# Optimization experiments

Hardware: AMD Instinct MI355X
Metric: run time of the kernel (lower is better)

The kernel has to match this reference:

```python
import jax, jax.numpy as jnp
import numpy as np
import math

B, S, D_EMB = 1, 4096, 768
N_HEADS, D_QKV = 12, 64
INV_TEMP = 1.0


def setup_inputs() -> dict:
    key = jax.random.key(0)
    ks = jax.random.split(key, 11)
    s = 0.02
    return {
        "q_in": jax.random.normal(ks[0], (B, S, D_EMB), jnp.float32),
        "k_in": jax.random.normal(ks[1], (B, S, D_EMB), jnp.float32),
        "v_in": jax.random.normal(ks[2], (B, S, D_EMB), jnp.float32),
        "W_q": jax.random.normal(ks[3], (D_EMB, N_HEADS * D_QKV), jnp.float32) * s,
        "b_q": jnp.zeros((N_HEADS * D_QKV,), jnp.float32),
        "W_k": jax.random.normal(ks[4], (D_EMB, N_HEADS * D_QKV), jnp.float32) * s,
        "b_k": jnp.zeros((N_HEADS * D_QKV,), jnp.float32),
        "W_v": jax.random.normal(ks[5], (D_EMB, N_HEADS * D_QKV), jnp.float32) * s,
        "b_v": jnp.zeros((N_HEADS * D_QKV,), jnp.float32),
        "W_o": jax.random.normal(ks[6], (N_HEADS * D_QKV, D_EMB), jnp.float32) * s,
        "b_o": jnp.zeros((D_EMB,), jnp.float32),
    }


def _split_heads(x):  # [B,S,H*D] -> [B,H,S,D]
    b, s, _ = x.shape
    return x.reshape(b, s, N_HEADS, D_QKV).transpose(0, 2, 1, 3)


def reference(q_in, k_in, v_in, W_q, b_q, W_k, b_k, W_v, b_v, W_o, b_o):
    q = _split_heads(q_in @ W_q + b_q)
    k = _split_heads(k_in @ W_k + b_k)
    v = _split_heads(v_in @ W_v + b_v)
    # full [B,H,S,S] score matrix (module materializes it for custom masking)
    scores = INV_TEMP * jnp.einsum('bhqd,bhkd->bhqk', q, k) / math.sqrt(D_QKV)
    attn = jax.nn.softmax(scores, axis=-1)
    out = jnp.einsum('bhqk,bhkd->bhqd', attn, v)  # [B,H,S,D]
    out = out.transpose(0, 2, 1, 3).reshape(q_in.shape[0], q_in.shape[1], N_HEADS * D_QKV)
    return out @ W_o + b_o
```

## Files before the change

### kernel.cpp

```cpp
#include <hip/hip_runtime.h>

#define S 4096
#define E 768
#define NH 12
#define DH 64
#define QSCALE (0.125f * 1.44269504f)

typedef __bf16 bf16;
typedef __bf16 bf16x4 __attribute__((ext_vector_type(4)));
typedef __bf16 bf16x8 __attribute__((ext_vector_type(8)));
typedef float  f32x4  __attribute__((ext_vector_type(4)));

__device__ __forceinline__ void async16(const bf16* g, bf16* l) {
  __builtin_amdgcn_global_load_lds(
      (const __attribute__((address_space(1))) void*)g,
      (__attribute__((address_space(3))) void*)l, 16, 0, 0);
}

__global__ __launch_bounds__(256) void cast3(const float* __restrict__ i0,
                                             const float* __restrict__ i1,
                                             const float* __restrict__ i2,
                                             bf16* __restrict__ o0,
                                             bf16* __restrict__ o1,
                                             bf16* __restrict__ o2) {
  const float* in = blockIdx.z == 0 ? i0 : (blockIdx.z == 1 ? i1 : i2);
  bf16* out = blockIdx.z == 0 ? o0 : (blockIdx.z == 1 ? o1 : o2);
  int i = (blockIdx.x * blockDim.x + threadIdx.x) * 4;
  float4 v = *(const float4*)(in + i);
  bf16x4 o = { (bf16)v.x, (bf16)v.y, (bf16)v.z, (bf16)v.w };
  *(bf16x4*)(out + i) = o;
}

__global__ __launch_bounds__(256) void transpose4(const float* __restrict__ w0,
                                                  const float* __restrict__ w1,
                                                  const float* __restrict__ w2,
                                                  const float* __restrict__ w3,
                                                  bf16* __restrict__ t0,
                                                  bf16* __restrict__ t1,
                                                  bf16* __restrict__ t2,
                                                  bf16* __restrict__ t3) {
  const float* W = blockIdx.z == 0 ? w0 : (blockIdx.z == 1 ? w1 : (blockIdx.z == 2 ? w2 : w3));
  bf16* Wt = blockIdx.z == 0 ? t0 : (blockIdx.z == 1 ? t1 : (blockIdx.z == 2 ? t2 : t3));
  __shared__ float t[32][33];
  const int tx = threadIdx.x, ty = threadIdx.y;
  const int x = blockIdx.x * 32 + tx;
  const int y0 = blockIdx.y * 32;
  for (int j = ty; j < 32; j += 8)
    t[j][tx] = W[(y0 + j) * E + x];
  __syncthreads();
  for (int j = ty; j < 32; j += 8)
    Wt[(blockIdx.x * 32 + j) * E + y0 + tx] = (bf16)t[tx][j];
}

template <int MODE>
__global__ __launch_bounds__(256) void gemm128(const bf16* __restrict__ A0,
                                               const bf16* __restrict__ A1,
                                               const bf16* __restrict__ A2,
                                               const bf16* __restrict__ B0,
                                               const bf16* __restrict__ B1,
                                               const bf16* __restrict__ B2,
                                               const float* __restrict__ bias0,
                                               const float* __restrict__ bias1,
                                               const float* __restrict__ bias2,
                                               void* __restrict__ C0,
                                               void* __restrict__ C1,
                                               void* __restrict__ C2) {
  __shared__ __align__(16) bf16 Asm[128 * 32];
  __shared__ __align__(16) bf16 Bsm[128 * 32];
  const int z = blockIdx.z;
  const bf16* A  = (MODE == 1 || z == 0) ? A0 : (z == 1 ? A1 : A2);
  const bf16* Bt = (MODE == 1 || z == 0) ? B0 : (z == 1 ? B1 : B2);
  const float* bias = (MODE == 1 || z == 0) ? bias0 : (z == 1 ? bias1 : bias2);

  const int tid = threadIdx.x;
  const int wv = tid >> 6, lane = tid & 63;
  const int quad = lane >> 4, l16 = lane & 15;
  const int m0 = blockIdx.x * 128, n0 = blockIdx.y * 128;
  const int wm = (wv >> 1) * 64, wn = (wv & 1) * 64;
  const int srow = lane >> 2, scol = (lane & 3) * 8;

  f32x4 acc[4][4] = {};

  for (int k0 = 0; k0 < E; k0 += 32) {
#pragma unroll
    for (int j = 0; j < 2; j++) {
      const int ch = wv * 2 + j;
      async16(&A[(size_t)(m0 + ch * 16 + srow) * E + k0 + scol], &Asm[ch * 512]);
      async16(&Bt[(size_t)(n0 + ch * 16 + srow) * E + k0 + scol], &Bsm[ch * 512]);
    }
    __syncthreads();
    bf16x8 af[4], bfv[4];
#pragma unroll
    for (int mi = 0; mi < 4; mi++)
      af[mi] = *(const bf16x8*)&Asm[(wm + mi * 16 + l16) * 32 + quad * 8];
#pragma unroll
    for (int ni = 0; ni < 4; ni++)
      bfv[ni] = *(const bf16x8*)&Bsm[(wn + ni * 16 + l16) * 32 + quad * 8];
#pragma unroll
    for (int mi = 0; mi < 4; mi++)
#pragma unroll
      for (int ni = 0; ni < 4; ni++)
        acc[mi][ni] = __builtin_amdgcn_mfma_f32_16x16x32_bf16(af[mi], bfv[ni], acc[mi][ni], 0, 0, 0);
    __syncthreads();
  }

#pragma unroll
  for (int mi = 0; mi < 4; mi++) {
    const int row0 = m0 + wm + mi * 16 + quad * 4;
#pragma unroll
    for (int ni = 0; ni < 4; ni++) {
      const int col = n0 + wn + ni * 16 + l16;
      const float bv = bias[col];
#pragma unroll
      for (int r = 0; r < 4; r++) {
        const int row = row0 + r;
        float v = acc[mi][ni][r] + bv;
        if (MODE == 1) {
          ((float*)C0)[(size_t)row * E + col] = v;
        } else {
          const int hh = col >> 6, d = col & 63;
          if (z == 0) {
            ((bf16*)C0)[(size_t)hh * S * DH + row * DH + d] = (bf16)(v * QSCALE);
          } else if (z == 1) {
            const int key = row;
            size_t idx = (size_t)hh * S * DH + (size_t)(key >> 6) * 4096 +
                         (size_t)((((key >> 4) & 3) * 2 + (d >> 5)) * 512) +
                         (size_t)((((d >> 3) & 3) * 16 + (key & 15)) * 8) + (d & 7);
            ((bf16*)C1)[idx] = (bf16)v;
          } else {
            const int key = row;
            size_t idx = (size_t)hh * S * DH + (size_t)(key >> 6) * 4096 +
                         (size_t)(((d >> 4) * 2 + ((key >> 5) & 1)) * 512) +
                         (size_t)((((key >> 3) & 3) * 16 + (d & 15)) * 8) + (key & 7);
            ((bf16*)C2)[idx] = (bf16)v;
          }
        }
      }
    }
  }
}

__global__ __launch_bounds__(256, 3) void attn(const bf16* __restrict__ Q,
                                               const bf16* __restrict__ Kf,
                                               const bf16* __restrict__ Vf,
                                               bf16* __restrict__ Op0,
                                               bf16* __restrict__ Op1,
                                               float* __restrict__ Lp) {
  __shared__ bf16 P[4][32][76];
  const int h = blockIdx.y, ks = blockIdx.z;
  const int tid = threadIdx.x;
  const int wave = tid >> 6, lane = tid & 63;
  const int quad = lane >> 4, l16 = lane & 15;
  const int q0 = blockIdx.x * 128 + wave * 32;

  const bf16* Qh  = Q  + (size_t)h * S * DH;
  const bf16* Kfh = Kf + (size_t)h * S * DH;
  const bf16* Vfh = Vf + (size_t)h * S * DH;
  bf16* Op = ks ? Op1 : Op0;

  bf16x8 aq[2][2];
#pragma unroll
  for (int mi = 0; mi < 2; mi++)
#pragma unroll
    for (int j = 0; j < 2; j++)
      aq[mi][j] = *(const bf16x8*)&Qh[(size_t)(q0 + mi * 16 + l16) * DH + j * 32 + quad * 8];

  f32x4 o[4][2] = {};
  float lacc[2][4] = {};

  const bf16* kptr = Kfh + (size_t)ks * 2048 * 64 + lane * 8;
  const bf16* vptr = Vfh + (size_t)ks * 2048 * 64 + lane * 8;

  for (int it = 0; it < 32; ++it, kptr += 4096, vptr += 4096) {
    bf16x8 kr[8];
#pragma unroll
    for (int i = 0; i < 8; i++) kr[i] = *(const bf16x8*)(kptr + i * 512);

#pragma unroll
    for (int mi = 0; mi < 2; mi++) {
      f32x4 sfr[4] = {};
#pragma unroll
      for (int nb = 0; nb < 4; nb++) {
        sfr[nb] = __builtin_amdgcn_mfma_f32_16x16x32_bf16(aq[mi][0], kr[nb * 2], sfr[nb], 0, 0, 0);
        sfr[nb] = __builtin_amdgcn_mfma_f32_16x16x32_bf16(aq[mi][1], kr[nb * 2 + 1], sfr[nb], 0, 0, 0);
      }
#pragma unroll
      for (int nb = 0; nb < 4; nb++)
#pragma unroll
        for (int r = 0; r < 4; r++) {
          float e = __builtin_exp2f(sfr[nb][r]);
          lacc[mi][r] += e;
          P[wave][mi * 16 + quad * 4 + r][nb * 16 + l16] = (bf16)e;
        }
    }

    bf16x8 vr[8];
#pragma unroll
    for (int i = 0; i < 8; i++) vr[i] = *(const bf16x8*)(vptr + i * 512);

    bf16x8 ap[2][2];
#pragma unroll
    for (int mi = 0; mi < 2; mi++)
#pragma unroll
      for (int j = 0; j < 2; j++)
        ap[mi][j] = *(const bf16x8*)&P[wave][mi * 16 + l16][j * 32 + quad * 8];

#pragma unroll
    for (int db = 0; db < 4; db++)
#pragma unroll
      for (int mi = 0; mi < 2; mi++) {
        o[db][mi] = __builtin_amdgcn_mfma_f32_16x16x32_bf16(ap[mi][0], vr[db * 2], o[db][mi], 0, 0, 0);
        o[db][mi] = __builtin_amdgcn_mfma_f32_16x16x32_bf16(ap[mi][1], vr[db * 2 + 1], o[db][mi], 0, 0, 0);
      }
  }

#pragma unroll
  for (int mi = 0; mi < 2; mi++)
#pragma unroll
    for (int r = 0; r < 4; r++) {
#pragma unroll
      for (int off = 8; off >= 1; off >>= 1)
        lacc[mi][r] += __shfl_xor(lacc[mi][r], off, 16);
    }

  float* Lph = Lp + (size_t)(ks * NH + h) * S;
  if (l16 == 0) {
#pragma unroll
    for (int mi = 0; mi < 2; mi++)
#pragma unroll
      for (int r = 0; r < 4; r++)
        Lph[q0 + mi * 16 + quad * 4 + r] = lacc[mi][r];
  }
#pragma unroll
  for (int db = 0; db < 4; db++) {
    const int d = db * 16 + l16;
#pragma unroll
    for (int mi = 0; mi < 2; mi++)
#pragma unroll
      for (int r = 0; r < 4; r++) {
        const int row = q0 + mi * 16 + quad * 4 + r;
        Op[(size_t)row * E + h * DH + d] = (bf16)o[db][mi][r];
      }
  }
}

__global__ __launch_bounds__(256) void combine(const bf16* __restrict__ Op0,
                                               const bf16* __restrict__ Op1,
                                               const float* __restrict__ Lp,
                                               bf16* __restrict__ Obf) {
  const int i8 = blockIdx.x * 256 + threadIdx.x;
  const size_t base = (size_t)i8 * 8;
  const int row = (int)(base / E), c = (int)(base % E);
  const int h = c >> 6;
  const float l = Lp[(size_t)h * S + row] + Lp[(size_t)(NH + h) * S + row];
  const float rl = 1.0f / l;
  bf16x8 a = *(const bf16x8*)(Op0 + base);
  bf16x8 b = *(const bf16x8*)(Op1 + base);
  bf16x8 o;
#pragma unroll
  for (int e = 0; e < 8; e++) o[e] = (bf16)(((float)a[e] + (float)b[e]) * rl);
  *(bf16x8*)(Obf + base) = o;
}

extern "C" void kernel_launch(void* const* d_in, const int* in_sizes, int n_in,
                              void* d_out, int out_size, void* d_ws, size_t ws_size,
                              hipStream_t stream) {
  (void)in_sizes; (void)n_in; (void)out_size; (void)ws_size;
  const float* q_in = (const float*)d_in[0];
  const float* k_in = (const float*)d_in[1];
  const float* v_in = (const float*)d_in[2];
  const float* W_q  = (const float*)d_in[3];
  const float* b_q  = (const float*)d_in[4];
  const float* W_k  = (const float*)d_in[5];
  const float* b_k  = (const float*)d_in[6];
  const float* W_v  = (const float*)d_in[7];
  const float* b_v  = (const float*)d_in[8];
  const float* W_o  = (const float*)d_in[9];
  const float* b_o  = (const float*)d_in[10];

  const size_t SE2 = (size_t)S * E * 2;
  const size_t EE2 = (size_t)E * E * 2;
  char* ws = (char*)d_ws;
  bf16* qb  = (bf16*)(ws);
  bf16* kb  = (bf16*)(ws + SE2);
  bf16* vb  = (bf16*)(ws + 2 * SE2);
  bf16* WqT = (bf16*)(ws + 3 * SE2);
  bf16* WkT = (bf16*)(ws + 3 * SE2 + EE2);
  bf16* WvT = (bf16*)(ws + 3 * SE2 + 2 * EE2);
  bf16* WoT = (bf16*)(ws + 3 * SE2 + 3 * EE2);
  bf16* Qh  = (bf16*)(ws + 3 * SE2 + 4 * EE2);
  bf16* Kf  = (bf16*)(ws + 4 * SE2 + 4 * EE2);
  bf16* Vf  = (bf16*)(ws + 5 * SE2 + 4 * EE2);
  bf16* Obf = (bf16*)(ws + 6 * SE2 + 4 * EE2);
  bf16* Op1   = qb;
  float* Lp   = (float*)WqT;

  cast3<<<dim3(S * E / 1024, 1, 3), 256, 0, stream>>>(q_in, k_in, v_in, qb, kb, vb);
  transpose4<<<dim3(24, 24, 4), dim3(32, 8), 0, stream>>>(W_q, W_k, W_v, W_o,
                                                          WqT, WkT, WvT, WoT);

  gemm128<0><<<dim3(S / 128, E / 128, 3), 256, 0, stream>>>(
      qb, kb, vb, WqT, WkT, WvT, b_q, b_k, b_v, Qh, Kf, Vf);

  attn<<<dim3(S / 128, NH, 2), 256, 0, stream>>>(Qh, Kf, Vf, Obf, Op1, Lp);

  combine<<<dim3(S * E / 2048), 256, 0, stream>>>(Obf, Op1, Lp, Obf);

  gemm128<1><<<dim3(S / 128, E / 128, 1), 256, 0, stream>>>(
      Obf, nullptr, nullptr, WoT, nullptr, nullptr, b_o, nullptr, nullptr,
      d_out, nullptr, nullptr);
}
```

Baseline: 253.1 us.

## Split attention keys four ways, stage QKV epilogue via LDS, smaller output GEMM

The attention key split grows from 2 to 4, which gives more blocks in the grid, and the occupancy hint rises to 4. The row-sum is now computed with an MFMA against a ones vector instead of per-element adds and shuffles. The QKV GEMM epilogue stages results through shared memory so the head and fragment layouts are written with vectorized 16-byte stores rather than scattered scalar stores. The output projection moves to a 64x64-tile GEMM so more blocks launch. In exchange, combine reads more partial buffers and the row-sum is taken from bf16-rounded P.

Result: faster. 239.4 us (-5.4%).

```diff
diff --git a/kernel.cpp b/kernel.cpp
--- a/kernel.cpp
+++ b/kernel.cpp
@@ -5,6 +5,7 @@
 #define NH 12
 #define DH 64
 #define QSCALE (0.125f * 1.44269504f)
+#define KSPLIT 4
 
 typedef __bf16 bf16;
 typedef __bf16 bf16x4 __attribute__((ext_vector_type(4)));
@@ -52,7 +53,6 @@
     Wt[(blockIdx.x * 32 + j) * E + y0 + tx] = (bf16)t[tx][j];
 }
 
-template <int MODE>
 __global__ __launch_bounds__(256) void gemm128(const bf16* __restrict__ A0,
                                                const bf16* __restrict__ A1,
                                                const bf16* __restrict__ A2,
@@ -62,15 +62,18 @@
                                                const float* __restrict__ bias0,
                                                const float* __restrict__ bias1,
                                                const float* __restrict__ bias2,
-                                               void* __restrict__ C0,
-                                               void* __restrict__ C1,
-                                               void* __restrict__ C2) {
-  __shared__ __align__(16) bf16 Asm[128 * 32];
-  __shared__ __align__(16) bf16 Bsm[128 * 32];
+                                               bf16* __restrict__ C0,
+                                               bf16* __restrict__ C1,
+                                               bf16* __restrict__ C2) {
+  __shared__ __align__(16) bf16 smem[128 * 136];
+  bf16* Asm = smem;
+  bf16* Bsm = smem + 4096;
+  bf16* Cs  = smem;
+
   const int z = blockIdx.z;
-  const bf16* A  = (MODE == 1 || z == 0) ? A0 : (z == 1 ? A1 : A2);
-  const bf16* Bt = (MODE == 1 || z == 0) ? B0 : (z == 1 ? B1 : B2);
-  const float* bias = (MODE == 1 || z == 0) ? bias0 : (z == 1 ? bias1 : bias2);
+  const bf16* A  = z == 0 ? A0 : (z == 1 ? A1 : A2);
+  const bf16* Bt = z == 0 ? B0 : (z == 1 ? B1 : B2);
+  const float* bias = z == 0 ? bias0 : (z == 1 ? bias1 : bias2);
 
   const int tid = threadIdx.x;
   const int wv = tid >> 6, lane = tid & 63;
@@ -104,47 +107,65 @@
     __syncthreads();
   }
 
+  const float scale = (z == 0) ? QSCALE : 1.0f;
 #pragma unroll
   for (int mi = 0; mi < 4; mi++) {
-    const int row0 = m0 + wm + mi * 16 + quad * 4;
 #pragma unroll
     for (int ni = 0; ni < 4; ni++) {
-      const int col = n0 + wn + ni * 16 + l16;
-      const float bv = bias[col];
+      const int nl = wn + ni * 16 + l16;
+      const float bv = bias[n0 + nl];
 #pragma unroll
       for (int r = 0; r < 4; r++) {
-        const int row = row0 + r;
-        float v = acc[mi][ni][r] + bv;
-        if (MODE == 1) {
-          ((float*)C0)[(size_t)row * E + col] = v;
-        } else {
-          const int hh = col >> 6, d = col & 63;
-          if (z == 0) {
-            ((bf16*)C0)[(size_t)hh * S * DH + row * DH + d] = (bf16)(v * QSCALE);
-          } else if (z == 1) {
-            const int key = row;
-            size_t idx = (size_t)hh * S * DH + (size_t)(key >> 6) * 4096 +
-                         (size_t)((((key >> 4) & 3) * 2 + (d >> 5)) * 512) +
-                         (size_t)((((d >> 3) & 3) * 16 + (key & 15)) * 8) + (d & 7);
-            ((bf16*)C1)[idx] = (bf16)v;
-          } else {
-            const int key = row;
-            size_t idx = (size_t)hh * S * DH + (size_t)(key >> 6) * 4096 +
-                         (size_t)(((d >> 4) * 2 + ((key >> 5) & 1)) * 512) +
-                         (size_t)((((key >> 3) & 3) * 16 + (d & 15)) * 8) + (key & 7);
-            ((bf16*)C2)[idx] = (bf16)v;
-          }
-        }
-      }
-    }
-  }
-}
-
-__global__ __launch_bounds__(256, 3) void attn(const bf16* __restrict__ Q,
+        const int ml = wm + mi * 16 + quad * 4 + r;
+        const float v = (acc[mi][ni][r] + bv) * scale;
+        if (z == 2) Cs[nl * 136 + ml] = (bf16)v;
+        else        Cs[ml * 136 + nl] = (bf16)v;
+      }
+    }
+  }
+  __syncthreads();
+
+  if (z == 0) {
+    const int e = lane & 7;
+#pragma unroll
+    for (int p = 0; p < 8; p++) {
+      const int hr = p * 32 + wv * 8 + (lane >> 3);
+      const int r = hr >> 1, hf = hr & 1;
+      bf16x8 c = *(const bf16x8*)&Cs[r * 136 + hf * 64 + e * 8];
+      *(bf16x8*)(C0 + (size_t)((n0 >> 6) + hf) * S * DH + (size_t)(m0 + r) * DH + e * 8) = c;
+    }
+  } else {
+    bf16* dst = (z == 1) ? C1 : C2;
+    const int quadc = lane >> 4, l16c = lane & 15;
+#pragma unroll
+    for (int p = 0; p < 8; p++) {
+      const int cid = p * 4 + wv;
+      const int reg = cid >> 3;
+      const int i = cid & 7;
+      const int h_l = reg >> 1, tile = reg & 1;
+      bf16x8 c;
+      if (z == 1) {
+        const int row = tile * 64 + (i >> 1) * 16 + l16c;
+        const int col = h_l * 64 + (i & 1) * 32 + quadc * 8;
+        c = *(const bf16x8*)&Cs[row * 136 + col];
+      } else {
+        const int nl = h_l * 64 + (i >> 1) * 16 + l16c;
+        const int ml = tile * 64 + (i & 1) * 32 + quadc * 8;
+        c = *(const bf16x8*)&Cs[nl * 136 + ml];
+      }
+      *(bf16x8*)(dst + (size_t)((n0 >> 6) + h_l) * S * DH +
+                 (size_t)((m0 >> 6) + tile) * 4096 + i * 512 + lane * 8) = c;
+    }
+  }
+}
+
+__global__ __launch_bounds__(256, 4) void attn(const bf16* __restrict__ Q,
                                                const bf16* __restrict__ Kf,
                                                const bf16* __restrict__ Vf,
                                                bf16* __restrict__ Op0,
                                                bf16* __restrict__ Op1,
+                                               bf16* __restrict__ Op2,
+                                               bf16* __restrict__ Op3,
                                                float* __restrict__ Lp) {
   __shared__ bf16 P[4][32][76];
   const int h = blockIdx.y, ks = blockIdx.z;
@@ -156,7 +177,7 @@
   const bf16* Qh  = Q  + (size_t)h * S * DH;
   const bf16* Kfh = Kf + (size_t)h * S * DH;
   const bf16* Vfh = Vf + (size_t)h * S * DH;
-  bf16* Op = ks ? Op1 : Op0;
+  bf16* Op = ks == 0 ? Op0 : (ks == 1 ? Op1 : (ks == 2 ? Op2 : Op3));
 
   bf16x8 aq[2][2];
 #pragma unroll
@@ -165,13 +186,17 @@
     for (int j = 0; j < 2; j++)
       aq[mi][j] = *(const bf16x8*)&Qh[(size_t)(q0 + mi * 16 + l16) * DH + j * 32 + quad * 8];
 
+  bf16x8 ones;
+#pragma unroll
+  for (int e = 0; e < 8; e++) ones[e] = (bf16)1.0f;
+
   f32x4 o[4][2] = {};
-  float lacc[2][4] = {};
-
-  const bf16* kptr = Kfh + (size_t)ks * 2048 * 64 + lane * 8;
-  const bf16* vptr = Vfh + (size_t)ks * 2048 * 64 + lane * 8;
-
-  for (int it = 0; it < 32; ++it, kptr += 4096, vptr += 4096) {
+  f32x4 ol[2] = {};
+
+  const bf16* kptr = Kfh + (size_t)ks * (S / KSPLIT) * DH + lane * 8;
+  const bf16* vptr = Vfh + (size_t)ks * (S / KSPLIT) * DH + lane * 8;
+
+  for (int it = 0; it < S / KSPLIT / 64; ++it, kptr += 4096, vptr += 4096) {
     bf16x8 kr[8];
 #pragma unroll
     for (int i = 0; i < 8; i++) kr[i] = *(const bf16x8*)(kptr + i * 512);
@@ -187,11 +212,8 @@
 #pragma unroll
       for (int nb = 0; nb < 4; nb++)
 #pragma unroll
-        for (int r = 0; r < 4; r++) {
-          float e = __builtin_exp2f(sfr[nb][r]);
-          lacc[mi][r] += e;
-          P[wave][mi * 16 + quad * 4 + r][nb * 16 + l16] = (bf16)e;
-        }
+        for (int r = 0; r < 4; r++)
+          P[wave][mi * 16 + quad * 4 + r][nb * 16 + l16] = (bf16)__builtin_exp2f(sfr[nb][r]);
     }
 
     bf16x8 vr[8];
@@ -205,6 +227,11 @@
       for (int j = 0; j < 2; j++)
         ap[mi][j] = *(const bf16x8*)&P[wave][mi * 16 + l16][j * 32 + quad * 8];
 
+#pragma unroll
+    for (int mi = 0; mi < 2; mi++) {
+      ol[mi] = __builtin_amdgcn_mfma_f32_16x16x32_bf16(ap[mi][0], ones, ol[mi], 0, 0, 0);
+      ol[mi] = __builtin_amdgcn_mfma_f32_16x16x32_bf16(ap[mi][1], ones, ol[mi], 0, 0, 0);
+    }
 #pragma unroll
     for (int db = 0; db < 4; db++)
 #pragma unroll
@@ -214,22 +241,13 @@
       }
   }
 
-#pragma unroll
-  for (int mi = 0; mi < 2; mi++)
-#pragma unroll
-    for (int r = 0; r < 4; r++) {
-#pragma unroll
-      for (int off = 8; off >= 1; off >>= 1)
-        lacc[mi][r] += __shfl_xor(lacc[mi][r], off, 16);
-    }
-
   float* Lph = Lp + (size_t)(ks * NH + h) * S;
   if (l16 == 0) {
 #pragma unroll
     for (int mi = 0; mi < 2; mi++)
 #pragma unroll
       for (int r = 0; r < 4; r++)
-        Lph[q0 + mi * 16 + quad * 4 + r] = lacc[mi][r];
+        Lph[q0 + mi * 16 + quad * 4 + r] = ol[mi][r];
   }
 #pragma unroll
   for (int db = 0; db < 4; db++) {
@@ -246,20 +264,64 @@
 
 __global__ __launch_bounds__(256) void combine(const bf16* __restrict__ Op0,
                                                const bf16* __restrict__ Op1,
+                                               const bf16* __restrict__ Op2,
+                                               const bf16* __restrict__ Op3,
                                                const float* __restrict__ Lp,
                                                bf16* __restrict__ Obf) {
   const int i8 = blockIdx.x * 256 + threadIdx.x;
   const size_t base = (size_t)i8 * 8;
   const int row = (int)(base / E), c = (int)(base % E);
   const int h = c >> 6;
-  const float l = Lp[(size_t)h * S + row] + Lp[(size_t)(NH + h) * S + row];
+  const float l = Lp[(size_t)h * S + row] + Lp[(size_t)(NH + h) * S + row] +
+                  Lp[(size_t)(2 * NH + h) * S + row] + Lp[(size_t)(3 * NH + h) * S + row];
   const float rl = 1.0f / l;
   bf16x8 a = *(const bf16x8*)(Op0 + base);
   bf16x8 b = *(const bf16x8*)(Op1 + base);
+  bf16x8 cc = *(const bf16x8*)(Op2 + base);
+  bf16x8 d = *(const bf16x8*)(Op3 + base);
   bf16x8 o;
 #pragma unroll
-  for (int e = 0; e < 8; e++) o[e] = (bf16)(((float)a[e] + (float)b[e]) * rl);
+  for (int e = 0; e < 8; e++)
+    o[e] = (bf16)((((float)a[e] + (float)b[e]) + ((float)cc[e] + (float)d[e])) * rl);
   *(bf16x8*)(Obf + base) = o;
+}
+
+__global__ __launch_bounds__(256) void gemm64(const bf16* __restrict__ A,
+                                              const bf16* __restrict__ Bt,
+                                              const float* __restrict__ bias,
+                                              float* __restrict__ C) {
+  __shared__ __align__(16) bf16 Asm[64 * 32];
+  __shared__ __align__(16) bf16 Bsm[64 * 32];
+  const int tid = threadIdx.x;
+  const int wv = tid >> 6, lane = tid & 63;
+  const int quad = lane >> 4, l16 = lane & 15;
+  const int m0 = blockIdx.x * 64, n0 = blockIdx.y * 64;
+  const int srow = lane >> 2, scol = (lane & 3) * 8;
+
+  f32x4 acc[4] = {};
+
+  for (int k0 = 0; k0 < E; k0 += 32) {
+    async16(&A[(size_t)(m0 + wv * 16 + srow) * E + k0 + scol], &Asm[wv * 512]);
+    async16(&Bt[(size_t)(n0 + wv * 16 + srow) * E + k0 + scol], &Bsm[wv * 512]);
+    __syncthreads();
+    bf16x8 af = *(const bf16x8*)&Asm[(wv * 16 + l16) * 32 + quad * 8];
+#pragma unroll
+    for (int ni = 0; ni < 4; ni++) {
+      bf16x8 bfr = *(const bf16x8*)&Bsm[(ni * 16 + l16) * 32 + quad * 8];
+      acc[ni] = __builtin_amdgcn_mfma_f32_16x16x32_bf16(af, bfr, acc[ni], 0, 0, 0);
+    }
+    __syncthreads();
+  }
+
+  const int row0 = m0 + wv * 16 + quad * 4;
+#pragma unroll
+  for (int ni = 0; ni < 4; ni++) {
+    const int col = n0 + ni * 16 + l16;
+    const float bv = bias[col];
+#pragma unroll
+    for (int r = 0; r < 4; r++)
+      C[(size_t)(row0 + r) * E + col] = acc[ni][r] + bv;
+  }
 }
 
 extern "C" void kernel_launch(void* const* d_in, const int* in_sizes, int n_in,
@@ -292,21 +354,21 @@
   bf16* Kf  = (bf16*)(ws + 4 * SE2 + 4 * EE2);
   bf16* Vf  = (bf16*)(ws + 5 * SE2 + 4 * EE2);
   bf16* Obf = (bf16*)(ws + 6 * SE2 + 4 * EE2);
-  bf16* Op1   = qb;
-  float* Lp   = (float*)WqT;
+  bf16* Op1 = qb;
+  bf16* Op2 = kb;
+  bf16* Op3 = vb;
+  float* Lp = (float*)WqT;
 
   cast3<<<dim3(S * E / 1024, 1, 3), 256, 0, stream>>>(q_in, k_in, v_in, qb, kb, vb);
   transpose4<<<dim3(24, 24, 4), dim3(32, 8), 0, stream>>>(W_q, W_k, W_v, W_o,
                                                           WqT, WkT, WvT, WoT);
 
-  gemm128<0><<<dim3(S / 128, E / 128, 3), 256, 0, stream>>>(
+  gemm128<<<dim3(S / 128, E / 128, 3), 256, 0, stream>>>(
       qb, kb, vb, WqT, WkT, WvT, b_q, b_k, b_v, Qh, Kf, Vf);
 
-  attn<<<dim3(S / 128, NH, 2), 256, 0, stream>>>(Qh, Kf, Vf, Obf, Op1, Lp);
-
-  combine<<<dim3(S * E / 2048), 256, 0, stream>>>(Obf, Op1, Lp, Obf);
-
-  gemm128<1><<<dim3(S / 128, E / 128, 1), 256, 0, stream>>>(
-      Obf, nullptr, nullptr, WoT, nullptr, nullptr, b_o, nullptr, nullptr,
-      d_out, nullptr, nullptr);
-}
+  attn<<<dim3(S / 128, NH, KSPLIT), 256, 0, stream>>>(Qh, Kf, Vf, Obf, Op1, Op2, Op3, Lp);
+
+  combine<<<dim3(S * E / 2048), 256, 0, stream>>>(Obf, Op1, Op2, Op3, Lp, Obf);
+
+  gemm64<<<dim3(S / 64, E / 64), 256, 0, stream>>>(Obf, WoT, b_o, (float*)d_out);
+}
```
